# Optimization experiments

Hardware: AMD Instinct MI355X
Metric: run time of the kernel (lower is better)

## Reference

```python
import jax, jax.numpy as jnp
import numpy as np

# pool sizes (must match init_kwargs)
N_FQK, N_FV, N_REL, N_VAL, N_KNOW = 512, 256, 128, 32, 256
K_FQK, K_FV, K_REL, K_VAL = 64, 32, 16, 3
D_MODEL, D_SPACE = 1024, 64
B, S = 8, 2048


def _topk_sparsify(w, k):
    # keep top-k entries per row, zero the rest (values unchanged)
    vals, idx = jax.lax.top_k(w, k)                      # [B,k]
    out = jnp.zeros_like(w)
    rows = jnp.arange(w.shape[0])[:, None]
    return out.at[rows, idx].set(vals), idx


def setup_inputs() -> dict:
    key = jax.random.key(0)
    k1, k2, k3, k4 = jax.random.split(key, 4)
    x = jax.random.normal(k1, (B, S, D_MODEL), dtype=jnp.float32)
    # importance: per-token weights normalized over sequence
    importance = jax.nn.softmax(jax.random.normal(k2, (B, S), dtype=jnp.float32), axis=-1)
    W = jax.random.normal(k3, (D_MODEL, D_SPACE), dtype=jnp.float32) * 0.02
    b = jnp.zeros((D_SPACE,), dtype=jnp.float32)
    total = N_FQK + N_FV + N_REL + N_VAL + N_KNOW
    neuron_emb = jax.random.normal(k4, (total, D_SPACE), dtype=jnp.float32) * 0.02
    return {"x": x, "importance": importance, "W": W, "b": b, "neuron_emb": neuron_emb}


def reference(x, importance, W, b, neuron_emb):
    # projection (dropout inactive in eval); normalized neuron embeddings
    h = x @ W + b                                         # [B,S,d_space]
    emb_n = neuron_emb / jnp.linalg.norm(neuron_emb, axis=-1, keepdims=True)
    all_logits = jnp.einsum('bsd,nd->bsn', h, emb_n)      # [B,S,N_total]

    e0 = N_FQK
    e1 = e0 + N_FV
    e2 = e1 + N_REL
    e3 = e2 + N_VAL

    def route(lo, hi):
        pref = jax.nn.softmax(all_logits[..., lo:hi], axis=-1)  # [B,S,n]
        w = jnp.einsum('bs,bsn->bn', importance, pref)          # [B,n]
        return pref, w

    _, w_qk = route(0, e0)
    _, idx_qk = jax.lax.top_k(w_qk, K_FQK)
    idx_qk = jnp.sort(idx_qk, axis=-1)

    _, w_v = route(e0, e1)
    _, idx_v = jax.lax.top_k(w_v, K_FV)
    idx_v = jnp.sort(idx_v, axis=-1)

    # relational Q and K share the same logit slice (eval: no excitability bonus)
    _, w_rQ = route(e1, e2)
    _, w_rK = route(e1, e2)
    rw_Q, _ = _topk_sparsify(w_rQ, K_REL)
    rw_K, _ = _topk_sparsify(w_rK, K_REL)

    _, w_val = route(e2, e3)
    vw, _ = _topk_sparsify(w_val, K_VAL)

    return idx_qk, idx_v, rw_Q, rw_K, vw, w_qk, w_v
```

## Files before the change

### kernel.cpp

```cpp
#include <hip/hip_runtime.h>
#include <hip/hip_bf16.h>
#include <math.h>

#define ROWS  16384
#define DM    1024
#define DS    64
#define NUSE  928
#define NPAD  960
#define NT    15

typedef __attribute__((ext_vector_type(8))) short bf16x8;
typedef __attribute__((ext_vector_type(4))) float f32x4;

static __device__ inline f32x4 mfma16(bf16x8 a, bf16x8 b, f32x4 c) {
    return __builtin_amdgcn_mfma_f32_16x16x32_bf16(a, b, c, 0, 0, 0);
}

static __device__ inline void bfsplit(float v, unsigned short& h, unsigned short& l) {
    unsigned u = __float_as_uint(v);
    unsigned hr = u + 0x7FFFu + ((u >> 16) & 1u);
    h = (unsigned short)(hr >> 16);
    float hf = __uint_as_float((unsigned)h << 16);
    float r = v - hf;
    unsigned ur = __float_as_uint(r);
    unsigned lr2 = ur + 0x7FFFu + ((ur >> 16) & 1u);
    l = (unsigned short)(lr2 >> 16);
}

#define OFF_EBH  0LL
#define OFF_EBL  122880LL
#define OFF_WBH  245760LL
#define OFF_WBL  376832LL
#define OFF_HP   507904LL
#define OFF_HBH  34062336LL
#define OFF_HBL  36159488LL
#define OFF_ZP   38256640LL
#define OFF_CF   39239680LL
#define OFF_WP   39501824LL

__global__ __launch_bounds__(256) void k_prep(const float* __restrict__ emb,
                                              unsigned short* __restrict__ ebh,
                                              unsigned short* __restrict__ ebl) {
    int n = blockIdx.x * 256 + threadIdx.x;
    if (n >= NPAD) return;
    if (n >= NUSE) {
        #pragma unroll
        for (int d = 0; d < DS; d++) {
            int kt = d >> 5, q = (d >> 3) & 3, j = d & 7;
            int a = ((kt * 4 + q) * NPAD + n) * 8 + j;
            ebh[a] = 0; ebl[a] = 0;
        }
        return;
    }
    float ss = 0.f;
    #pragma unroll
    for (int d = 0; d < DS; d++) { float v = emb[n * DS + d]; ss = fmaf(v, v, ss); }
    float inv = 1.0f / sqrtf(ss);
    #pragma unroll
    for (int d = 0; d < DS; d++) {
        float v = emb[n * DS + d] * inv;
        unsigned short h, l; bfsplit(v, h, l);
        int kt = d >> 5, q = (d >> 3) & 3, j = d & 7;
        int a = ((kt * 4 + q) * NPAD + n) * 8 + j;
        ebh[a] = h; ebl[a] = l;
    }
}

__global__ __launch_bounds__(256) void k_prepw(const float* __restrict__ W,
                                               unsigned short* __restrict__ wbh,
                                               unsigned short* __restrict__ wbl) {
    int idx = blockIdx.x * 256 + threadIdx.x;
    int ktg = idx >> 6, n = idx & 63;
    #pragma unroll
    for (int q = 0; q < 4; q++) {
        #pragma unroll
        for (int j = 0; j < 8; j++) {
            int k = ktg * 32 + q * 8 + j;
            float v = W[k * DS + n];
            unsigned short h, l; bfsplit(v, h, l);
            int a = ((ktg * 4 + q) * 64 + n) * 8 + j;
            wbh[a] = h; wbl[a] = l;
        }
    }
}

__global__ __launch_bounds__(256) void k_hmm(const float* __restrict__ x,
                                             const unsigned short* __restrict__ wbh,
                                             const unsigned short* __restrict__ wbl,
                                             float* __restrict__ hpart) {
    __shared__ unsigned short Ah[4 * 4 * 64 * 8];
    __shared__ unsigned short Al[4 * 4 * 64 * 8];
    const int tid = threadIdx.x;
    const int rc = blockIdx.x, g = blockIdx.y;
    const long long row0 = (long long)rc * 64;
    const int k0 = g * 128;

    {
        int r = tid >> 2, cg = tid & 3;
        const float* xp = &x[(row0 + r) * DM + k0 + cg * 32];
        #pragma unroll
        for (int u = 0; u < 8; u++) {
            float4 v = *(const float4*)&xp[u * 4];
            int q = u >> 1, j0 = (u & 1) * 4;
            int base = ((cg * 4 + q) * 64 + r) * 8 + j0;
            unsigned short h0, l0, h1, l1, h2, l2, h3, l3;
            bfsplit(v.x, h0, l0); bfsplit(v.y, h1, l1);
            bfsplit(v.z, h2, l2); bfsplit(v.w, h3, l3);
            uint2 ph; ph.x = (unsigned)h0 | ((unsigned)h1 << 16); ph.y = (unsigned)h2 | ((unsigned)h3 << 16);
            uint2 pl; pl.x = (unsigned)l0 | ((unsigned)l1 << 16); pl.y = (unsigned)l2 | ((unsigned)l3 << 16);
            *(uint2*)&Ah[base] = ph;
            *(uint2*)&Al[base] = pl;
        }
    }
    __syncthreads();

    const int w = tid >> 6, lane = tid & 63, q = lane >> 4, lm = lane & 15;
    f32x4 acc[4];
    #pragma unroll
    for (int f = 0; f < 4; f++) { acc[f].x = 0.f; acc[f].y = 0.f; acc[f].z = 0.f; acc[f].w = 0.f; }

    #pragma unroll
    for (int kt = 0; kt < 4; kt++) {
        const bf16x8 a_h = *(const bf16x8*)&Ah[((kt * 4 + q) * 64 + w * 16 + lm) * 8];
        const bf16x8 a_l = *(const bf16x8*)&Al[((kt * 4 + q) * 64 + w * 16 + lm) * 8];
        const int ktg = g * 4 + kt;
        #pragma unroll
        for (int f = 0; f < 4; f++) {
            int ba = ((ktg * 4 + q) * 64 + f * 16 + lm) * 8;
            bf16x8 b_h = *(const bf16x8*)&wbh[ba];
            bf16x8 b_l = *(const bf16x8*)&wbl[ba];
            acc[f] = mfma16(a_h, b_h, acc[f]);
            acc[f] = mfma16(a_h, b_l, acc[f]);
            acc[f] = mfma16(a_l, b_h, acc[f]);
        }
    }

    float* hp = &hpart[((long long)g * ROWS + row0) * 64];
    #pragma unroll
    for (int f = 0; f < 4; f++) {
        #pragma unroll
        for (int t = 0; t < 4; t++) {
            hp[(w * 16 + q * 4 + t) * 64 + f * 16 + lm] = acc[f][t];
        }
    }
}

__global__ __launch_bounds__(256) void k_hadd(const float* __restrict__ hpart,
                                              const float* __restrict__ bias,
                                              unsigned short* __restrict__ hbh,
                                              unsigned short* __restrict__ hbl) {
    int i = blockIdx.x * 256 + threadIdx.x;
    int gr = i >> 3, qq = i & 7;
    int d0 = qq * 8;
    float4 s0 = *(const float4*)&bias[d0];
    float4 s1 = *(const float4*)&bias[d0 + 4];
    #pragma unroll
    for (int g = 0; g < 8; g++) {
        const float* p = &hpart[((long long)g * ROWS + gr) * 64 + d0];
        float4 a = *(const float4*)&p[0];
        float4 b = *(const float4*)&p[4];
        s0.x += a.x; s0.y += a.y; s0.z += a.z; s0.w += a.w;
        s1.x += b.x; s1.y += b.y; s1.z += b.z; s1.w += b.w;
    }
    unsigned short h[8], l[8];
    bfsplit(s0.x, h[0], l[0]); bfsplit(s0.y, h[1], l[1]);
    bfsplit(s0.z, h[2], l[2]); bfsplit(s0.w, h[3], l[3]);
    bfsplit(s1.x, h[4], l[4]); bfsplit(s1.y, h[5], l[5]);
    bfsplit(s1.z, h[6], l[6]); bfsplit(s1.w, h[7], l[7]);
    int rc = gr >> 6, lr = gr & 63;
    int kt = qq >> 2, q = qq & 3;
    int base = (((rc * 2 + kt) * 4 + q) * 64 + lr) * 8;
    uint4 ph, pl;
    ph.x = (unsigned)h[0] | ((unsigned)h[1] << 16); ph.y = (unsigned)h[2] | ((unsigned)h[3] << 16);
    ph.z = (unsigned)h[4] | ((unsigned)h[5] << 16); ph.w = (unsigned)h[6] | ((unsigned)h[7] << 16);
    pl.x = (unsigned)l[0] | ((unsigned)l[1] << 16); pl.y = (unsigned)l[2] | ((unsigned)l[3] << 16);
    pl.z = (unsigned)l[4] | ((unsigned)l[5] << 16); pl.w = (unsigned)l[6] | ((unsigned)l[7] << 16);
    *(uint4*)&hbh[base] = ph;
    *(uint4*)&hbl[base] = pl;
}

static __device__ inline void logits_gemm(const unsigned short* __restrict__ hbh,
                                          const unsigned short* __restrict__ hbl,
                                          const unsigned short* __restrict__ ebh,
                                          const unsigned short* __restrict__ ebl,
                                          int rc, int nt, int w, int q, int lm,
                                          f32x4 acc[4]) {
    #pragma unroll
    for (int f = 0; f < 4; f++) { acc[f].x = 0.f; acc[f].y = 0.f; acc[f].z = 0.f; acc[f].w = 0.f; }
    #pragma unroll
    for (int kt = 0; kt < 2; kt++) {
        int ab = (((rc * 2 + kt) * 4 + q) * 64 + w * 16 + lm) * 8;
        const bf16x8 a_h = *(const bf16x8*)&hbh[ab];
        const bf16x8 a_l = *(const bf16x8*)&hbl[ab];
        #pragma unroll
        for (int f = 0; f < 4; f++) {
            int bb = ((kt * 4 + q) * NPAD + nt * 64 + f * 16 + lm) * 8;
            bf16x8 b_h = *(const bf16x8*)&ebh[bb];
            bf16x8 b_l = *(const bf16x8*)&ebl[bb];
            acc[f] = mfma16(a_h, b_h, acc[f]);
            acc[f] = mfma16(a_h, b_l, acc[f]);
            acc[f] = mfma16(a_l, b_h, acc[f]);
        }
    }
}

__global__ __launch_bounds__(256) void k_z(const unsigned short* __restrict__ hbh,
                                           const unsigned short* __restrict__ hbl,
                                           const unsigned short* __restrict__ ebh,
                                           const unsigned short* __restrict__ ebl,
                                           float* __restrict__ zpart) {
    const int rc = blockIdx.x, nt = blockIdx.y;
    const int tid = threadIdx.x, w = tid >> 6, lane = tid & 63, q = lane >> 4, lm = lane & 15;
    f32x4 acc[4];
    logits_gemm(hbh, hbl, ebh, ebl, rc, nt, w, q, lm, acc);

    float s0 = 0.f, s1 = 0.f, s2 = 0.f, s3 = 0.f;
    #pragma unroll
    for (int f = 0; f < 4; f++) {
        if (nt * 64 + f * 16 < NUSE) {
            s0 += __expf(acc[f][0]); s1 += __expf(acc[f][1]);
            s2 += __expf(acc[f][2]); s3 += __expf(acc[f][3]);
        }
    }
    #pragma unroll
    for (int off = 1; off < 16; off <<= 1) {
        s0 += __shfl_xor(s0, off); s1 += __shfl_xor(s1, off);
        s2 += __shfl_xor(s2, off); s3 += __shfl_xor(s3, off);
    }
    if (lm < 4) {
        float sv = (lm == 0) ? s0 : (lm == 1) ? s1 : (lm == 2) ? s2 : s3;
        zpart[(long long)nt * ROWS + rc * 64 + w * 16 + q * 4 + lm] = sv;
    }
}

__global__ __launch_bounds__(256) void k_coef(const float* __restrict__ imp,
                                              const float* __restrict__ zpart,
                                              float* __restrict__ coef) {
    int r = blockIdx.x * 256 + threadIdx.x;
    float z0 = 0.f, z1 = 0.f, z2 = 0.f;
    #pragma unroll
    for (int t = 0; t < 8; t++)  z0 += zpart[(long long)t * ROWS + r];
    #pragma unroll
    for (int t = 8; t < 12; t++) z1 += zpart[(long long)t * ROWS + r];
    z2 = zpart[12LL * ROWS + r] + zpart[13LL * ROWS + r];
    float z3 = zpart[14LL * ROWS + r];
    float im = imp[r];
    float4 c; c.x = im / z0; c.y = im / z1; c.z = im / z2; c.w = im / z3;
    *(float4*)&coef[(long long)r * 4] = c;
}

__global__ __launch_bounds__(256) void k_pw(const unsigned short* __restrict__ hbh,
                                            const unsigned short* __restrict__ hbl,
                                            const unsigned short* __restrict__ ebh,
                                            const unsigned short* __restrict__ ebl,
                                            const float* __restrict__ coef,
                                            float* __restrict__ wpart) {
    const int rc = blockIdx.x, nt = blockIdx.y;
    const int tid = threadIdx.x, w = tid >> 6, lane = tid & 63, q = lane >> 4, lm = lane & 15;
    f32x4 acc[4];
    logits_gemm(hbh, hbl, ebh, ebl, rc, nt, w, q, lm, acc);

    const int sl = (nt < 8) ? 0 : (nt < 12) ? 1 : (nt < 14) ? 2 : 3;
    const int rbase = rc * 64 + w * 16 + q * 4;
    float c0 = coef[(long long)(rbase + 0) * 4 + sl];
    float c1 = coef[(long long)(rbase + 1) * 4 + sl];
    float c2 = coef[(long long)(rbase + 2) * 4 + sl];
    float c3 = coef[(long long)(rbase + 3) * 4 + sl];

    float wsum[4];
    #pragma unroll
    for (int f = 0; f < 4; f++) {
        wsum[f] = c0 * __expf(acc[f][0]) + c1 * __expf(acc[f][1])
                + c2 * __expf(acc[f][2]) + c3 * __expf(acc[f][3]);
        wsum[f] += __shfl_xor(wsum[f], 16);
        wsum[f] += __shfl_xor(wsum[f], 32);
    }
    __shared__ float wbuf[4][64];
    if (lane < 16) {
        #pragma unroll
        for (int f = 0; f < 4; f++) wbuf[w][f * 16 + lane] = wsum[f];
    }
    __syncthreads();
    if (tid < 64) {
        int n = nt * 64 + tid;
        if (n < NUSE) {
            wpart[(long long)rc * NPAD + n] =
                (wbuf[0][tid] + wbuf[1][tid]) + (wbuf[2][tid] + wbuf[3][tid]);
        }
    }
}

__global__ __launch_bounds__(512) void k_out(const float* __restrict__ wpart,
                                             float* __restrict__ out) {
    const int b = blockIdx.x;
    const int tid = threadIdx.x;
    __shared__ float w_s[NUSE];
    __shared__ int   rk[NUSE];

    for (int n = tid; n < NUSE; n += 512) {
        float s = 0.f;
        #pragma unroll 4
        for (int c = 0; c < 32; c++)
            s += wpart[(long long)(b * 32 + c) * NPAD + n];
        w_s[n] = s;
        if (n < 512)      out[3072 + (long long)b * 512 + n] = s;
        else if (n < 768) out[7168 + (long long)b * 256 + (n - 512)] = s;
    }
    __syncthreads();

    for (int n = tid; n < NUSE; n += 512) {
        int lo, hi;
        if (n < 512)      { lo = 0;   hi = 512; }
        else if (n < 768) { lo = 512; hi = 768; }
        else if (n < 896) { lo = 768; hi = 896; }
        else              { lo = 896; hi = NUSE; }
        float wn = w_s[n];
        int r = 0;
        for (int m = lo; m < hi; m++) {
            float wm = w_s[m];
            r += (wm > wn) || ((wm == wn) && (m < n));
        }
        rk[n] = r;
    }
    __syncthreads();

    if (tid < 512) {
        int n = tid;
        if (rk[n] < 64) {
            int pos = 0;
            for (int m = 0; m < n; m++) pos += (rk[m] < 64) ? 1 : 0;
            out[(long long)b * 64 + pos] = (float)n;
        }
    }
    if (tid < 256) {
        int n = 512 + tid;
        if (rk[n] < 32) {
            int pos = 0;
            for (int m = 512; m < n; m++) pos += (rk[m] < 32) ? 1 : 0;
            out[512 + (long long)b * 32 + pos] = (float)tid;
        }
    }
    if (tid < 128) {
        int n = 768 + tid;
        float v = (rk[n] < 16) ? w_s[n] : 0.f;
        out[768 + (long long)b * 128 + tid] = v;
        out[1792 + (long long)b * 128 + tid] = v;
    }
    if (tid < 32) {
        int n = 896 + tid;
        float v = (rk[n] < 3) ? w_s[n] : 0.f;
        out[2816 + (long long)b * 32 + tid] = v;
    }
}

extern "C" void kernel_launch(void* const* d_in, const int* in_sizes, int n_in,
                              void* d_out, int out_size, void* d_ws, size_t ws_size,
                              hipStream_t stream) {
    const float* x    = (const float*)d_in[0];
    const float* imp  = (const float*)d_in[1];
    const float* W    = (const float*)d_in[2];
    const float* bias = (const float*)d_in[3];
    const float* emb  = (const float*)d_in[4];

    char* ws = (char*)d_ws;
    unsigned short* ebh = (unsigned short*)(ws + OFF_EBH);
    unsigned short* ebl = (unsigned short*)(ws + OFF_EBL);
    unsigned short* wbh = (unsigned short*)(ws + OFF_WBH);
    unsigned short* wbl = (unsigned short*)(ws + OFF_WBL);
    float* hpart        = (float*)(ws + OFF_HP);
    unsigned short* hbh = (unsigned short*)(ws + OFF_HBH);
    unsigned short* hbl = (unsigned short*)(ws + OFF_HBL);
    float* zpart        = (float*)(ws + OFF_ZP);
    float* coef         = (float*)(ws + OFF_CF);
    float* wpart        = (float*)(ws + OFF_WP);
    float* out          = (float*)d_out;

    k_prep<<<4, 256, 0, stream>>>(emb, ebh, ebl);
    k_prepw<<<8, 256, 0, stream>>>(W, wbh, wbl);
    k_hmm<<<dim3(256, 8), 256, 0, stream>>>(x, wbh, wbl, hpart);
    k_hadd<<<512, 256, 0, stream>>>(hpart, bias, hbh, hbl);
    k_z<<<dim3(256, NT), 256, 0, stream>>>(hbh, hbl, ebh, ebl, zpart);
    k_coef<<<64, 256, 0, stream>>>(imp, zpart, coef);
    k_pw<<<dim3(256, NT), 256, 0, stream>>>(hbh, hbl, ebh, ebl, coef, wpart);
    k_out<<<8, 512, 0, stream>>>(wpart, out);
}
```

Before: 190.3 us.

## Fuse logits, softmax normalizer and weighted reduction into one kernel

Merges the two weight-prep kernels, halves the split-K count of the projection GEMM with register prefetch of the second K chunk, and fuses the partial-sum add, logits GEMM, softmax normalizer and importance-weighted reduction into one per-row-chunk kernel. Exponentials are stored as fp16 in shared memory so the normalizer and weighted sum come from a single logits GEMM pass. This removes the duplicated logits GEMM and several intermediate global buffers and launches. In exchange it uses a large shared-memory footprint per 1024-thread block and adds fp16 rounding of the exp values, which risks accuracy and overflow for large logits.

Result: faster. 167.0 us (-12.3%).

```diff
diff --git a/kernel.cpp b/kernel.cpp
--- a/kernel.cpp
+++ b/kernel.cpp
@@ -1,5 +1,6 @@
 #include <hip/hip_runtime.h>
 #include <hip/hip_bf16.h>
+#include <hip/hip_fp16.h>
 #include <math.h>
 
 #define ROWS  16384
@@ -32,98 +33,98 @@
 #define OFF_WBH  245760LL
 #define OFF_WBL  376832LL
 #define OFF_HP   507904LL
-#define OFF_HBH  34062336LL
-#define OFF_HBL  36159488LL
-#define OFF_ZP   38256640LL
-#define OFF_CF   39239680LL
-#define OFF_WP   39501824LL
+#define OFF_WP   17285120LL
 
 __global__ __launch_bounds__(256) void k_prep(const float* __restrict__ emb,
+                                              const float* __restrict__ W,
                                               unsigned short* __restrict__ ebh,
-                                              unsigned short* __restrict__ ebl) {
-    int n = blockIdx.x * 256 + threadIdx.x;
-    if (n >= NPAD) return;
-    if (n >= NUSE) {
+                                              unsigned short* __restrict__ ebl,
+                                              unsigned short* __restrict__ wbh,
+                                              unsigned short* __restrict__ wbl) {
+    if (blockIdx.x < 4) {
+        int n = blockIdx.x * 256 + threadIdx.x;
+        if (n >= NPAD) return;
+        if (n >= NUSE) {
+            #pragma unroll
+            for (int d = 0; d < DS; d++) {
+                int kt = d >> 5, q = (d >> 3) & 3, j = d & 7;
+                int a = ((kt * 4 + q) * NPAD + n) * 8 + j;
+                ebh[a] = 0; ebl[a] = 0;
+            }
+            return;
+        }
+        float ss = 0.f;
+        #pragma unroll
+        for (int d = 0; d < DS; d++) { float v = emb[n * DS + d]; ss = fmaf(v, v, ss); }
+        float inv = 1.0f / sqrtf(ss);
         #pragma unroll
         for (int d = 0; d < DS; d++) {
+            float v = emb[n * DS + d] * inv;
+            unsigned short h, l; bfsplit(v, h, l);
             int kt = d >> 5, q = (d >> 3) & 3, j = d & 7;
             int a = ((kt * 4 + q) * NPAD + n) * 8 + j;
-            ebh[a] = 0; ebl[a] = 0;
-        }
-        return;
-    }
-    float ss = 0.f;
-    #pragma unroll
-    for (int d = 0; d < DS; d++) { float v = emb[n * DS + d]; ss = fmaf(v, v, ss); }
-    float inv = 1.0f / sqrtf(ss);
-    #pragma unroll
-    for (int d = 0; d < DS; d++) {
-        float v = emb[n * DS + d] * inv;
-        unsigned short h, l; bfsplit(v, h, l);
-        int kt = d >> 5, q = (d >> 3) & 3, j = d & 7;
-        int a = ((kt * 4 + q) * NPAD + n) * 8 + j;
-        ebh[a] = h; ebl[a] = l;
-    }
-}
-
-__global__ __launch_bounds__(256) void k_prepw(const float* __restrict__ W,
-                                               unsigned short* __restrict__ wbh,
-                                               unsigned short* __restrict__ wbl) {
-    int idx = blockIdx.x * 256 + threadIdx.x;
-    int ktg = idx >> 6, n = idx & 63;
-    #pragma unroll
-    for (int q = 0; q < 4; q++) {
-        #pragma unroll
-        for (int j = 0; j < 8; j++) {
-            int k = ktg * 32 + q * 8 + j;
-            float v = W[k * DS + n];
-            unsigned short h, l; bfsplit(v, h, l);
-            int a = ((ktg * 4 + q) * 64 + n) * 8 + j;
-            wbh[a] = h; wbl[a] = l;
-        }
-    }
-}
-
-__global__ __launch_bounds__(256) void k_hmm(const float* __restrict__ x,
-                                             const unsigned short* __restrict__ wbh,
-                                             const unsigned short* __restrict__ wbl,
-                                             float* __restrict__ hpart) {
+            ebh[a] = h; ebl[a] = l;
+        }
+    } else {
+        int idx = (blockIdx.x - 4) * 256 + threadIdx.x;
+        int ktg = idx >> 6, n = idx & 63;
+        #pragma unroll
+        for (int q = 0; q < 4; q++) {
+            #pragma unroll
+            for (int j = 0; j < 8; j++) {
+                int k = ktg * 32 + q * 8 + j;
+                float v = W[k * DS + n];
+                unsigned short h, l; bfsplit(v, h, l);
+                int a = ((ktg * 4 + q) * 64 + n) * 8 + j;
+                wbh[a] = h; wbl[a] = l;
+            }
+        }
+    }
+}
+
+__global__ __launch_bounds__(256, 4) void k_hmm(const float* __restrict__ x,
+                                                const unsigned short* __restrict__ wbh,
+                                                const unsigned short* __restrict__ wbl,
+                                                float* __restrict__ hpart) {
     __shared__ unsigned short Ah[4 * 4 * 64 * 8];
     __shared__ unsigned short Al[4 * 4 * 64 * 8];
     const int tid = threadIdx.x;
     const int rc = blockIdx.x, g = blockIdx.y;
     const long long row0 = (long long)rc * 64;
-    const int k0 = g * 128;
-
-    {
-        int r = tid >> 2, cg = tid & 3;
-        const float* xp = &x[(row0 + r) * DM + k0 + cg * 32];
-        #pragma unroll
-        for (int u = 0; u < 8; u++) {
-            float4 v = *(const float4*)&xp[u * 4];
-            int q = u >> 1, j0 = (u & 1) * 4;
-            int base = ((cg * 4 + q) * 64 + r) * 8 + j0;
-            unsigned short h0, l0, h1, l1, h2, l2, h3, l3;
-            bfsplit(v.x, h0, l0); bfsplit(v.y, h1, l1);
-            bfsplit(v.z, h2, l2); bfsplit(v.w, h3, l3);
-            uint2 ph; ph.x = (unsigned)h0 | ((unsigned)h1 << 16); ph.y = (unsigned)h2 | ((unsigned)h3 << 16);
-            uint2 pl; pl.x = (unsigned)l0 | ((unsigned)l1 << 16); pl.y = (unsigned)l2 | ((unsigned)l3 << 16);
-            *(uint2*)&Ah[base] = ph;
-            *(uint2*)&Al[base] = pl;
-        }
-    }
-    __syncthreads();
+
+    const int sr = tid >> 2, scg = tid & 3;
+    const float* xrow = &x[(row0 + sr) * DM + g * 256 + scg * 32];
 
     const int w = tid >> 6, lane = tid & 63, q = lane >> 4, lm = lane & 15;
     f32x4 acc[4];
     #pragma unroll
     for (int f = 0; f < 4; f++) { acc[f].x = 0.f; acc[f].y = 0.f; acc[f].z = 0.f; acc[f].w = 0.f; }
+
+    float4 pf[8];
+    #pragma unroll
+    for (int u = 0; u < 8; u++) pf[u] = *(const float4*)&xrow[u * 4];
+    #pragma unroll
+    for (int u = 0; u < 8; u++) {
+        int qq = u >> 1, j0 = (u & 1) * 4;
+        int base = ((scg * 4 + qq) * 64 + sr) * 8 + j0;
+        unsigned short h0, l0, h1, l1, h2, l2, h3, l3;
+        bfsplit(pf[u].x, h0, l0); bfsplit(pf[u].y, h1, l1);
+        bfsplit(pf[u].z, h2, l2); bfsplit(pf[u].w, h3, l3);
+        uint2 ph; ph.x = (unsigned)h0 | ((unsigned)h1 << 16); ph.y = (unsigned)h2 | ((unsigned)h3 << 16);
+        uint2 pl; pl.x = (unsigned)l0 | ((unsigned)l1 << 16); pl.y = (unsigned)l2 | ((unsigned)l3 << 16);
+        *(uint2*)&Ah[base] = ph;
+        *(uint2*)&Al[base] = pl;
+    }
+    __syncthreads();
+
+    #pragma unroll
+    for (int u = 0; u < 8; u++) pf[u] = *(const float4*)&xrow[128 + u * 4];
 
     #pragma unroll
     for (int kt = 0; kt < 4; kt++) {
         const bf16x8 a_h = *(const bf16x8*)&Ah[((kt * 4 + q) * 64 + w * 16 + lm) * 8];
         const bf16x8 a_l = *(const bf16x8*)&Al[((kt * 4 + q) * 64 + w * 16 + lm) * 8];
-        const int ktg = g * 4 + kt;
+        const int ktg = g * 8 + kt;
         #pragma unroll
         for (int f = 0; f < 4; f++) {
             int ba = ((ktg * 4 + q) * 64 + f * 16 + lm) * 8;
@@ -134,159 +135,176 @@
             acc[f] = mfma16(a_l, b_h, acc[f]);
         }
     }
-
-    float* hp = &hpart[((long long)g * ROWS + row0) * 64];
-    #pragma unroll
-    for (int f = 0; f < 4; f++) {
-        #pragma unroll
-        for (int t = 0; t < 4; t++) {
-            hp[(w * 16 + q * 4 + t) * 64 + f * 16 + lm] = acc[f][t];
-        }
-    }
-}
-
-__global__ __launch_bounds__(256) void k_hadd(const float* __restrict__ hpart,
-                                              const float* __restrict__ bias,
-                                              unsigned short* __restrict__ hbh,
-                                              unsigned short* __restrict__ hbl) {
-    int i = blockIdx.x * 256 + threadIdx.x;
-    int gr = i >> 3, qq = i & 7;
-    int d0 = qq * 8;
-    float4 s0 = *(const float4*)&bias[d0];
-    float4 s1 = *(const float4*)&bias[d0 + 4];
-    #pragma unroll
-    for (int g = 0; g < 8; g++) {
-        const float* p = &hpart[((long long)g * ROWS + gr) * 64 + d0];
-        float4 a = *(const float4*)&p[0];
-        float4 b = *(const float4*)&p[4];
-        s0.x += a.x; s0.y += a.y; s0.z += a.z; s0.w += a.w;
-        s1.x += b.x; s1.y += b.y; s1.z += b.z; s1.w += b.w;
-    }
-    unsigned short h[8], l[8];
-    bfsplit(s0.x, h[0], l[0]); bfsplit(s0.y, h[1], l[1]);
-    bfsplit(s0.z, h[2], l[2]); bfsplit(s0.w, h[3], l[3]);
-    bfsplit(s1.x, h[4], l[4]); bfsplit(s1.y, h[5], l[5]);
-    bfsplit(s1.z, h[6], l[6]); bfsplit(s1.w, h[7], l[7]);
-    int rc = gr >> 6, lr = gr & 63;
-    int kt = qq >> 2, q = qq & 3;
-    int base = (((rc * 2 + kt) * 4 + q) * 64 + lr) * 8;
-    uint4 ph, pl;
-    ph.x = (unsigned)h[0] | ((unsigned)h[1] << 16); ph.y = (unsigned)h[2] | ((unsigned)h[3] << 16);
-    ph.z = (unsigned)h[4] | ((unsigned)h[5] << 16); ph.w = (unsigned)h[6] | ((unsigned)h[7] << 16);
-    pl.x = (unsigned)l[0] | ((unsigned)l[1] << 16); pl.y = (unsigned)l[2] | ((unsigned)l[3] << 16);
-    pl.z = (unsigned)l[4] | ((unsigned)l[5] << 16); pl.w = (unsigned)l[6] | ((unsigned)l[7] << 16);
-    *(uint4*)&hbh[base] = ph;
-    *(uint4*)&hbl[base] = pl;
-}
-
-static __device__ inline void logits_gemm(const unsigned short* __restrict__ hbh,
-                                          const unsigned short* __restrict__ hbl,
-                                          const unsigned short* __restrict__ ebh,
-                                          const unsigned short* __restrict__ ebl,
-                                          int rc, int nt, int w, int q, int lm,
-                                          f32x4 acc[4]) {
-    #pragma unroll
-    for (int f = 0; f < 4; f++) { acc[f].x = 0.f; acc[f].y = 0.f; acc[f].z = 0.f; acc[f].w = 0.f; }
-    #pragma unroll
-    for (int kt = 0; kt < 2; kt++) {
-        int ab = (((rc * 2 + kt) * 4 + q) * 64 + w * 16 + lm) * 8;
-        const bf16x8 a_h = *(const bf16x8*)&hbh[ab];
-        const bf16x8 a_l = *(const bf16x8*)&hbl[ab];
+    __syncthreads();
+
+    #pragma unroll
+    for (int u = 0; u < 8; u++) {
+        int qq = u >> 1, j0 = (u & 1) * 4;
+        int base = ((scg * 4 + qq) * 64 + sr) * 8 + j0;
+        unsigned short h0, l0, h1, l1, h2, l2, h3, l3;
+        bfsplit(pf[u].x, h0, l0); bfsplit(pf[u].y, h1, l1);
+        bfsplit(pf[u].z, h2, l2); bfsplit(pf[u].w, h3, l3);
+        uint2 ph; ph.x = (unsigned)h0 | ((unsigned)h1 << 16); ph.y = (unsigned)h2 | ((unsigned)h3 << 16);
+        uint2 pl; pl.x = (unsigned)l0 | ((unsigned)l1 << 16); pl.y = (unsigned)l2 | ((unsigned)l3 << 16);
+        *(uint2*)&Ah[base] = ph;
+        *(uint2*)&Al[base] = pl;
+    }
+    __syncthreads();
+
+    #pragma unroll
+    for (int kt = 0; kt < 4; kt++) {
+        const bf16x8 a_h = *(const bf16x8*)&Ah[((kt * 4 + q) * 64 + w * 16 + lm) * 8];
+        const bf16x8 a_l = *(const bf16x8*)&Al[((kt * 4 + q) * 64 + w * 16 + lm) * 8];
+        const int ktg = g * 8 + 4 + kt;
         #pragma unroll
         for (int f = 0; f < 4; f++) {
-            int bb = ((kt * 4 + q) * NPAD + nt * 64 + f * 16 + lm) * 8;
-            bf16x8 b_h = *(const bf16x8*)&ebh[bb];
-            bf16x8 b_l = *(const bf16x8*)&ebl[bb];
+            int ba = ((ktg * 4 + q) * 64 + f * 16 + lm) * 8;
+            bf16x8 b_h = *(const bf16x8*)&wbh[ba];
+            bf16x8 b_l = *(const bf16x8*)&wbl[ba];
             acc[f] = mfma16(a_h, b_h, acc[f]);
             acc[f] = mfma16(a_h, b_l, acc[f]);
             acc[f] = mfma16(a_l, b_h, acc[f]);
         }
     }
-}
-
-__global__ __launch_bounds__(256) void k_z(const unsigned short* __restrict__ hbh,
-                                           const unsigned short* __restrict__ hbl,
-                                           const unsigned short* __restrict__ ebh,
-                                           const unsigned short* __restrict__ ebl,
-                                           float* __restrict__ zpart) {
-    const int rc = blockIdx.x, nt = blockIdx.y;
-    const int tid = threadIdx.x, w = tid >> 6, lane = tid & 63, q = lane >> 4, lm = lane & 15;
-    f32x4 acc[4];
-    logits_gemm(hbh, hbl, ebh, ebl, rc, nt, w, q, lm, acc);
-
-    float s0 = 0.f, s1 = 0.f, s2 = 0.f, s3 = 0.f;
+
+    float* hp = &hpart[((long long)g * ROWS + row0) * 64];
     #pragma unroll
     for (int f = 0; f < 4; f++) {
-        if (nt * 64 + f * 16 < NUSE) {
-            s0 += __expf(acc[f][0]); s1 += __expf(acc[f][1]);
-            s2 += __expf(acc[f][2]); s3 += __expf(acc[f][3]);
-        }
-    }
-    #pragma unroll
-    for (int off = 1; off < 16; off <<= 1) {
-        s0 += __shfl_xor(s0, off); s1 += __shfl_xor(s1, off);
-        s2 += __shfl_xor(s2, off); s3 += __shfl_xor(s3, off);
-    }
-    if (lm < 4) {
-        float sv = (lm == 0) ? s0 : (lm == 1) ? s1 : (lm == 2) ? s2 : s3;
-        zpart[(long long)nt * ROWS + rc * 64 + w * 16 + q * 4 + lm] = sv;
-    }
-}
-
-__global__ __launch_bounds__(256) void k_coef(const float* __restrict__ imp,
-                                              const float* __restrict__ zpart,
-                                              float* __restrict__ coef) {
-    int r = blockIdx.x * 256 + threadIdx.x;
-    float z0 = 0.f, z1 = 0.f, z2 = 0.f;
-    #pragma unroll
-    for (int t = 0; t < 8; t++)  z0 += zpart[(long long)t * ROWS + r];
-    #pragma unroll
-    for (int t = 8; t < 12; t++) z1 += zpart[(long long)t * ROWS + r];
-    z2 = zpart[12LL * ROWS + r] + zpart[13LL * ROWS + r];
-    float z3 = zpart[14LL * ROWS + r];
-    float im = imp[r];
-    float4 c; c.x = im / z0; c.y = im / z1; c.z = im / z2; c.w = im / z3;
-    *(float4*)&coef[(long long)r * 4] = c;
-}
-
-__global__ __launch_bounds__(256) void k_pw(const unsigned short* __restrict__ hbh,
-                                            const unsigned short* __restrict__ hbl,
-                                            const unsigned short* __restrict__ ebh,
-                                            const unsigned short* __restrict__ ebl,
-                                            const float* __restrict__ coef,
-                                            float* __restrict__ wpart) {
-    const int rc = blockIdx.x, nt = blockIdx.y;
-    const int tid = threadIdx.x, w = tid >> 6, lane = tid & 63, q = lane >> 4, lm = lane & 15;
-    f32x4 acc[4];
-    logits_gemm(hbh, hbl, ebh, ebl, rc, nt, w, q, lm, acc);
-
-    const int sl = (nt < 8) ? 0 : (nt < 12) ? 1 : (nt < 14) ? 2 : 3;
-    const int rbase = rc * 64 + w * 16 + q * 4;
-    float c0 = coef[(long long)(rbase + 0) * 4 + sl];
-    float c1 = coef[(long long)(rbase + 1) * 4 + sl];
-    float c2 = coef[(long long)(rbase + 2) * 4 + sl];
-    float c3 = coef[(long long)(rbase + 3) * 4 + sl];
-
-    float wsum[4];
-    #pragma unroll
-    for (int f = 0; f < 4; f++) {
-        wsum[f] = c0 * __expf(acc[f][0]) + c1 * __expf(acc[f][1])
-                + c2 * __expf(acc[f][2]) + c3 * __expf(acc[f][3]);
-        wsum[f] += __shfl_xor(wsum[f], 16);
-        wsum[f] += __shfl_xor(wsum[f], 32);
-    }
-    __shared__ float wbuf[4][64];
-    if (lane < 16) {
-        #pragma unroll
-        for (int f = 0; f < 4; f++) wbuf[w][f * 16 + lane] = wsum[f];
-    }
-    __syncthreads();
+        #pragma unroll
+        for (int t = 0; t < 4; t++) {
+            hp[(w * 16 + q * 4 + t) * 64 + f * 16 + lm] = acc[f][t];
+        }
+    }
+}
+
+__global__ __launch_bounds__(1024, 4) void k_zpw(const float* __restrict__ hpart,
+                                                 const float* __restrict__ bias,
+                                                 const unsigned short* __restrict__ ebh,
+                                                 const unsigned short* __restrict__ ebl,
+                                                 const float* __restrict__ imp,
+                                                 float* __restrict__ wpart) {
+    __shared__ __align__(16) unsigned short Ph[NPAD * 72];
+    __shared__ __align__(16) unsigned short Ah[2 * 4 * 64 * 8];
+    __shared__ __align__(16) unsigned short Al[2 * 4 * 64 * 8];
+    __shared__ float zslot[4][4][64];
+    __shared__ float coefL[64 * 4];
+
+    const int tid = threadIdx.x;
+    const int rc = blockIdx.x;
+
+    if (tid < 1024) ((float*)zslot)[tid] = 0.f;
+
+    {
+        int r = tid >> 4, seg = tid & 15;
+        int col = seg * 4;
+        float4 s = *(const float4*)&bias[col];
+        #pragma unroll
+        for (int g = 0; g < 4; g++) {
+            float4 a = *(const float4*)&hpart[((long long)g * ROWS + rc * 64 + r) * 64 + col];
+            s.x += a.x; s.y += a.y; s.z += a.z; s.w += a.w;
+        }
+        unsigned short h0, l0, h1, l1, h2, l2, h3, l3;
+        bfsplit(s.x, h0, l0); bfsplit(s.y, h1, l1);
+        bfsplit(s.z, h2, l2); bfsplit(s.w, h3, l3);
+        int kt = seg >> 3, q = (seg >> 1) & 3, j0 = (seg & 1) * 4;
+        int base = ((kt * 4 + q) * 64 + r) * 8 + j0;
+        uint2 ph; ph.x = (unsigned)h0 | ((unsigned)h1 << 16); ph.y = (unsigned)h2 | ((unsigned)h3 << 16);
+        uint2 pl; pl.x = (unsigned)l0 | ((unsigned)l1 << 16); pl.y = (unsigned)l2 | ((unsigned)l3 << 16);
+        *(uint2*)&Ah[base] = ph;
+        *(uint2*)&Al[base] = pl;
+    }
+    __syncthreads();
+
+    const int w = tid >> 6, lane = tid & 63, q = lane >> 4, lm = lane & 15;
+    const int rw = w & 3, wg = w >> 2;
+
+    bf16x8 a_h[2], a_l[2];
+    #pragma unroll
+    for (int kt = 0; kt < 2; kt++) {
+        int ab = ((kt * 4 + q) * 64 + rw * 16 + lm) * 8;
+        a_h[kt] = *(const bf16x8*)&Ah[ab];
+        a_l[kt] = *(const bf16x8*)&Al[ab];
+    }
+
+    #pragma unroll
+    for (int v = 0; v < 4; v++) {
+        int nt = wg + v * 4;
+        if (nt > 14) continue;
+        f32x4 acc[4];
+        #pragma unroll
+        for (int f = 0; f < 4; f++) { acc[f].x = 0.f; acc[f].y = 0.f; acc[f].z = 0.f; acc[f].w = 0.f; }
+        #pragma unroll
+        for (int kt = 0; kt < 2; kt++) {
+            #pragma unroll
+            for (int f = 0; f < 4; f++) {
+                int bb = ((kt * 4 + q) * NPAD + nt * 64 + f * 16 + lm) * 8;
+                bf16x8 b_h = *(const bf16x8*)&ebh[bb];
+                bf16x8 b_l = *(const bf16x8*)&ebl[bb];
+                acc[f] = mfma16(a_h[kt], b_h, acc[f]);
+                acc[f] = mfma16(a_h[kt], b_l, acc[f]);
+                acc[f] = mfma16(a_l[kt], b_h, acc[f]);
+            }
+        }
+        const int sl = (nt < 8) ? 0 : (nt < 12) ? 1 : (nt < 14) ? 2 : 3;
+        float s0 = 0.f, s1 = 0.f, s2 = 0.f, s3 = 0.f;
+        #pragma unroll
+        for (int f = 0; f < 4; f++) {
+            float e0 = __expf(acc[f][0]);
+            float e1 = __expf(acc[f][1]);
+            float e2 = __expf(acc[f][2]);
+            float e3 = __expf(acc[f][3]);
+            int n = nt * 64 + f * 16 + lm;
+            unsigned short p0 = __half_as_ushort(__float2half(e0));
+            unsigned short p1 = __half_as_ushort(__float2half(e1));
+            unsigned short p2 = __half_as_ushort(__float2half(e2));
+            unsigned short p3 = __half_as_ushort(__float2half(e3));
+            uint2 pk; pk.x = (unsigned)p0 | ((unsigned)p1 << 16); pk.y = (unsigned)p2 | ((unsigned)p3 << 16);
+            *(uint2*)&Ph[n * 72 + rw * 16 + q * 4] = pk;
+            if (nt * 64 + f * 16 < NUSE) {
+                s0 += e0; s1 += e1; s2 += e2; s3 += e3;
+            }
+        }
+        #pragma unroll
+        for (int off = 1; off < 16; off <<= 1) {
+            s0 += __shfl_xor(s0, off); s1 += __shfl_xor(s1, off);
+            s2 += __shfl_xor(s2, off); s3 += __shfl_xor(s3, off);
+        }
+        if (lm < 4) {
+            float sv = (lm == 0) ? s0 : (lm == 1) ? s1 : (lm == 2) ? s2 : s3;
+            zslot[wg][sl][rw * 16 + q * 4 + lm] += sv;
+        }
+    }
+    __syncthreads();
+
     if (tid < 64) {
-        int n = nt * 64 + tid;
-        if (n < NUSE) {
-            wpart[(long long)rc * NPAD + n] =
-                (wbuf[0][tid] + wbuf[1][tid]) + (wbuf[2][tid] + wbuf[3][tid]);
-        }
+        int r = tid;
+        float im = imp[rc * 64 + r];
+        #pragma unroll
+        for (int sl = 0; sl < 4; sl++) {
+            float Z = zslot[0][sl][r] + zslot[1][sl][r] + zslot[2][sl][r] + zslot[3][sl][r];
+            coefL[r * 4 + sl] = im / Z;
+        }
+    }
+    __syncthreads();
+
+    if (tid < NUSE) {
+        int n = tid;
+        int sl = (n < 512) ? 0 : (n < 768) ? 1 : (n < 896) ? 2 : 3;
+        float acc = 0.f;
+        #pragma unroll
+        for (int rb = 0; rb < 8; rb++) {
+            uint4 pk = *(const uint4*)&Ph[n * 72 + rb * 8];
+            const unsigned pv[4] = {pk.x, pk.y, pk.z, pk.w};
+            #pragma unroll
+            for (int u = 0; u < 4; u++) {
+                float v0 = __half2float(__ushort_as_half((unsigned short)(pv[u] & 0xFFFF)));
+                float v1 = __half2float(__ushort_as_half((unsigned short)(pv[u] >> 16)));
+                int row = rb * 8 + u * 2;
+                acc = fmaf(coefL[(row + 0) * 4 + sl], v0, acc);
+                acc = fmaf(coefL[(row + 1) * 4 + sl], v1, acc);
+            }
+        }
+        wpart[(long long)rc * NPAD + n] = acc;
     }
 }
 
@@ -368,19 +386,11 @@
     unsigned short* wbh = (unsigned short*)(ws + OFF_WBH);
     unsigned short* wbl = (unsigned short*)(ws + OFF_WBL);
     float* hpart        = (float*)(ws + OFF_HP);
-    unsigned short* hbh = (unsigned short*)(ws + OFF_HBH);
-    unsigned short* hbl = (unsigned short*)(ws + OFF_HBL);
-    float* zpart        = (float*)(ws + OFF_ZP);
-    float* coef         = (float*)(ws + OFF_CF);
     float* wpart        = (float*)(ws + OFF_WP);
     float* out          = (float*)d_out;
 
-    k_prep<<<4, 256, 0, stream>>>(emb, ebh, ebl);
-    k_prepw<<<8, 256, 0, stream>>>(W, wbh, wbl);
-    k_hmm<<<dim3(256, 8), 256, 0, stream>>>(x, wbh, wbl, hpart);
-    k_hadd<<<512, 256, 0, stream>>>(hpart, bias, hbh, hbl);
-    k_z<<<dim3(256, NT), 256, 0, stream>>>(hbh, hbl, ebh, ebl, zpart);
-    k_coef<<<64, 256, 0, stream>>>(imp, zpart, coef);
-    k_pw<<<dim3(256, NT), 256, 0, stream>>>(hbh, hbl, ebh, ebl, coef, wpart);
+    k_prep<<<12, 256, 0, stream>>>(emb, W, ebh, ebl, wbh, wbl);
+    k_hmm<<<dim3(256, 4), 256, 0, stream>>>(x, wbh, wbl, hpart);
+    k_zpw<<<256, 1024, 0, stream>>>(hpart, bias, ebh, ebl, imp, wpart);
     k_out<<<8, 512, 0, stream>>>(wpart, out);
 }
```
